# Kernel optimization log

Measured on AMD Instinct MI355X. Metric: run time of the kernel, lower is better.

Reference implementation:

```python
import jax, jax.numpy as jnp
import numpy as np

# DISTANA prediction-kernel step, fused per spatial node:
#   pre  = tanh(x @ W_pre)                       (B,N,9) -> (B,N,4)
#   net  = pre @ W_lstm + old_h                  (B,N,16) recurrent state feeds gating
#   CIFG-style LSTM cell (single gate matrix, as dictated by the (4,16) lstm_weights):
#     i        = sigmoid(net)
#     g        = tanh(net)
#     new_cell = (1-i)*old_cell + i*g
#     new_h    = tanh(new_cell)
#   y   = tanh(new_h @ W_post)                   (B,N,16) -> (B,N,9)

B, N = 128, 4096          # batch, number of prediction kernels (64x64 grid)
IN, PRE, CELLS, OUT = 9, 4, 16, 9


def setup_inputs() -> dict:
    key = jax.random.key(0)
    k = jax.random.split(key, 6)
    stdv = 1.0 / float(np.sqrt(CELLS))  # reset_parameters(): uniform(-stdv, stdv)
    return {
        "input": jax.random.normal(k[0], (B, N, IN, 1), dtype=jnp.float32),
        "pre_weights": jax.random.uniform(k[1], (IN, PRE), jnp.float32, -stdv, stdv),
        "lstm_weights": jax.random.uniform(k[2], (PRE, CELLS), jnp.float32, -stdv, stdv),
        "post_weights": jax.random.uniform(k[3], (CELLS, OUT), jnp.float32, -stdv, stdv),
        "old_h": jax.random.normal(k[4], (B, N, CELLS), dtype=jnp.float32),
        "old_cell": jax.random.normal(k[5], (B, N, CELLS), dtype=jnp.float32),
    }


def reference(input, pre_weights, lstm_weights, post_weights, old_h, old_cell):
    x = input[..., 0]                                  # (B,N,9) drop trailing singleton
    pre = jnp.tanh(jnp.einsum("bni,ip->bnp", x, pre_weights))        # (B,N,4)
    net = jnp.einsum("bnp,pc->bnc", pre, lstm_weights) + old_h       # (B,N,16)
    i = jax.nn.sigmoid(net)
    g = jnp.tanh(net)
    new_cell = (1.0 - i) * old_cell + i * g                          # (B,N,16)
    new_h = jnp.tanh(new_cell)                                       # (B,N,16)
    y = jnp.tanh(jnp.einsum("bnc,co->bno", new_h, post_weights))     # (B,N,9)
    return y, new_h, new_cell


if __name__ == "__main__":
    out = jax.jit(reference)(**setup_inputs())
    print([o.shape for o in out])
```

## Files before the change

kernel.cpp:

```cpp
#include <hip/hip_runtime.h>
#include <math.h>


#define NNODES 524288
#define IN_DIM 9
#define CELLS 16
#define OUT_DIM 9
#define TPB 256
#define NPB 64
#define NBLK (NNODES / NPB)
#define NXCD 8

typedef float f32x4 __attribute__((ext_vector_type(4)));

__device__ __forceinline__ float fast_rcp(float x) {
    return __builtin_amdgcn_rcpf(x);
}

__device__ __forceinline__ float fast_tanh(float x) {
    x = fminf(fmaxf(x, -15.f), 15.f);
    float e = __expf(2.f * x);
    return (e - 1.f) * fast_rcp(e + 1.f);
}

__device__ __forceinline__ float qsum(float v) {
    v += __int_as_float(__builtin_amdgcn_ds_swizzle(__float_as_int(v), 0x041F));
    v += __int_as_float(__builtin_amdgcn_ds_swizzle(__float_as_int(v), 0x081F));
    return v;
}

__global__ __launch_bounds__(TPB) void distana_quad_kernel(
    const float* __restrict__ input,
    const float* __restrict__ w_pre,
    const float* __restrict__ w_lstm,
    const float* __restrict__ w_post,
    const float* __restrict__ old_h,
    const float* __restrict__ old_cell,
    float* __restrict__ y,
    float* __restrict__ new_h,
    float* __restrict__ new_cell)
{
    __shared__ float sWpre[64];
    __shared__ float sWl[64];
    __shared__ float sWp[144];

    const int t   = threadIdx.x;
    const int bid = blockIdx.x;
    const int swz  = (bid & (NXCD - 1)) * (NBLK / NXCD) + (bid >> 3);
    const int node = swz * NPB + (t >> 2);
    const int sub  = t & 3;

    const float* hp = old_h    + (size_t)node * CELLS + sub * 4;
    const float* cp = old_cell + (size_t)node * CELLS + sub * 4;
    f32x4 h = *(const f32x4*)hp;
    f32x4 c = *(const f32x4*)cp;

    const float* xp = input + (size_t)node * IN_DIM;
    f32x4 xl = {0.f, 0.f, 0.f, 0.f};
    if (sub == 0)      { xl[0] = xp[0]; xl[1] = xp[1]; xl[2] = xp[2]; xl[3] = xp[3]; }
    else if (sub == 1) { xl[0] = xp[4]; xl[1] = xp[5]; xl[2] = xp[6]; xl[3] = xp[7]; }
    else if (sub == 2) { xl[0] = xp[8]; }

    if (t < 64)  sWpre[t] = (t < 36) ? w_pre[t] : 0.f;
    if (t < 64)  sWl[t]   = w_lstm[t];
    if (t < 144) sWp[t]   = w_post[t];
    __syncthreads();

    float pre[4];
    #pragma unroll
    for (int p = 0; p < 4; ++p) {
        float s = 0.f;
        #pragma unroll
        for (int k = 0; k < 4; ++k)
            s = fmaf(xl[k], sWpre[(sub * 4 + k) * 4 + p], s);
        pre[p] = fast_tanh(qsum(s));
    }

    f32x4 nh, nc;
    #pragma unroll
    for (int j = 0; j < 4; ++j) {
        const int cc = sub * 4 + j;
        float s = h[j];
        #pragma unroll
        for (int p = 0; p < 4; ++p)
            s = fmaf(pre[p], sWl[p * CELLS + cc], s);
        s = fminf(fmaxf(s, -15.f), 15.f);
        float e  = __expf(s);
        float e2 = e * e;
        float a  = 1.f + e;
        float b  = 1.f + e2;
        float r  = fast_rcp(a * b);
        float ig = e * b * r;
        float g  = (e2 - 1.f) * a * r;
        float v  = fmaf(ig, g - c[j], c[j]);
        nc[j] = v;
        nh[j] = fast_tanh(v);
    }
    *(f32x4*)(new_h    + (size_t)node * CELLS + sub * 4) = nh;
    *(f32x4*)(new_cell + (size_t)node * CELLS + sub * 4) = nc;

    float py[OUT_DIM];
    #pragma unroll
    for (int o = 0; o < OUT_DIM; ++o) {
        float s = 0.f;
        #pragma unroll
        for (int j = 0; j < 4; ++j)
            s = fmaf(nh[j], sWp[(sub * 4 + j) * OUT_DIM + o], s);
        py[o] = qsum(s);
    }
    float* yo = y + (size_t)node * OUT_DIM;
    if (sub == 0) {
        yo[0] = fast_tanh(py[0]); yo[1] = fast_tanh(py[1]);
        yo[2] = fast_tanh(py[2]); yo[3] = fast_tanh(py[3]);
    } else if (sub == 1) {
        yo[4] = fast_tanh(py[4]); yo[5] = fast_tanh(py[5]);
        yo[6] = fast_tanh(py[6]); yo[7] = fast_tanh(py[7]);
    } else if (sub == 2) {
        yo[8] = fast_tanh(py[8]);
    }
}

extern "C" void kernel_launch(void* const* d_in, const int* in_sizes, int n_in,
                              void* d_out, int out_size, void* d_ws, size_t ws_size,
                              hipStream_t stream) {
    const float* input    = (const float*)d_in[0];
    const float* w_pre    = (const float*)d_in[1];
    const float* w_lstm   = (const float*)d_in[2];
    const float* w_post   = (const float*)d_in[3];
    const float* old_h    = (const float*)d_in[4];
    const float* old_cell = (const float*)d_in[5];

    float* out = (float*)d_out;
    float* yp       = out;
    float* new_h    = out + (size_t)NNODES * OUT_DIM;
    float* new_cell = new_h + (size_t)NNODES * CELLS;

    dim3 grid(NBLK), block(TPB);
    distana_quad_kernel<<<grid, block, 0, stream>>>(
        input, w_pre, w_lstm, w_post, old_h, old_cell, yp, new_h, new_cell);
}
```

Measured before the change: 33.38 us.

## Use DPP quad reductions, nontemporal stores, drop clamps, reorder loads

Replaces ds_swizzle quad reductions with DPP row permutes, writes all outputs with nontemporal stores, and removes clamping before several exp calls. It also moves the weight loads to shared memory ahead of the global h/c loads and spreads the y writes as 3/3/3 across lanes. The aim is lower instruction latency and less cache pollution on a store-heavy, memory-bound kernel. Without the clamps, exp can overflow to inf for large inputs, and (inf-1)*rcp(inf+1) can produce NaN in tanh.

```diff
diff --git a/kernel.cpp b/kernel.cpp
--- a/kernel.cpp
+++ b/kernel.cpp
@@ -17,15 +17,20 @@
     return __builtin_amdgcn_rcpf(x);
 }
 
-__device__ __forceinline__ float fast_tanh(float x) {
-    x = fminf(fmaxf(x, -15.f), 15.f);
+__device__ __forceinline__ float tanh_nc(float x) {
     float e = __expf(2.f * x);
     return (e - 1.f) * fast_rcp(e + 1.f);
 }
 
+__device__ __forceinline__ float fast_tanh(float x) {
+    return tanh_nc(fminf(fmaxf(x, -15.f), 15.f));
+}
+
 __device__ __forceinline__ float qsum(float v) {
-    v += __int_as_float(__builtin_amdgcn_ds_swizzle(__float_as_int(v), 0x041F));
-    v += __int_as_float(__builtin_amdgcn_ds_swizzle(__float_as_int(v), 0x081F));
+    int a = __builtin_amdgcn_update_dpp(0, __float_as_int(v), 0xB1, 0xF, 0xF, true);
+    v += __int_as_float(a);
+    int b = __builtin_amdgcn_update_dpp(0, __float_as_int(v), 0x4E, 0xF, 0xF, true);
+    v += __int_as_float(b);
     return v;
 }
 
@@ -50,10 +55,9 @@
     const int node = swz * NPB + (t >> 2);
     const int sub  = t & 3;
 
-    const float* hp = old_h    + (size_t)node * CELLS + sub * 4;
-    const float* cp = old_cell + (size_t)node * CELLS + sub * 4;
-    f32x4 h = *(const f32x4*)hp;
-    f32x4 c = *(const f32x4*)cp;
+    if (t < 64)  sWpre[t] = (t < 36) ? w_pre[t] : 0.f;
+    if (t < 64)  sWl[t]   = w_lstm[t];
+    if (t < 144) sWp[t]   = w_post[t];
 
     const float* xp = input + (size_t)node * IN_DIM;
     f32x4 xl = {0.f, 0.f, 0.f, 0.f};
@@ -61,9 +65,11 @@
     else if (sub == 1) { xl[0] = xp[4]; xl[1] = xp[5]; xl[2] = xp[6]; xl[3] = xp[7]; }
     else if (sub == 2) { xl[0] = xp[8]; }
 
-    if (t < 64)  sWpre[t] = (t < 36) ? w_pre[t] : 0.f;
-    if (t < 64)  sWl[t]   = w_lstm[t];
-    if (t < 144) sWp[t]   = w_post[t];
+    const float* hp = old_h    + (size_t)node * CELLS + sub * 4;
+    const float* cp = old_cell + (size_t)node * CELLS + sub * 4;
+    f32x4 h = *(const f32x4*)hp;
+    f32x4 c = *(const f32x4*)cp;
+
     __syncthreads();
 
     float pre[4];
@@ -84,7 +90,6 @@
         #pragma unroll
         for (int p = 0; p < 4; ++p)
             s = fmaf(pre[p], sWl[p * CELLS + cc], s);
-        s = fminf(fmaxf(s, -15.f), 15.f);
         float e  = __expf(s);
         float e2 = e * e;
         float a  = 1.f + e;
@@ -94,10 +99,10 @@
         float g  = (e2 - 1.f) * a * r;
         float v  = fmaf(ig, g - c[j], c[j]);
         nc[j] = v;
-        nh[j] = fast_tanh(v);
+        nh[j] = tanh_nc(v);
     }
-    *(f32x4*)(new_h    + (size_t)node * CELLS + sub * 4) = nh;
-    *(f32x4*)(new_cell + (size_t)node * CELLS + sub * 4) = nc;
+    __builtin_nontemporal_store(nh, (f32x4*)(new_h    + (size_t)node * CELLS + sub * 4));
+    __builtin_nontemporal_store(nc, (f32x4*)(new_cell + (size_t)node * CELLS + sub * 4));
 
     float py[OUT_DIM];
     #pragma unroll
@@ -110,13 +115,17 @@
     }
     float* yo = y + (size_t)node * OUT_DIM;
     if (sub == 0) {
-        yo[0] = fast_tanh(py[0]); yo[1] = fast_tanh(py[1]);
-        yo[2] = fast_tanh(py[2]); yo[3] = fast_tanh(py[3]);
+        __builtin_nontemporal_store(tanh_nc(py[0]), yo + 0);
+        __builtin_nontemporal_store(tanh_nc(py[1]), yo + 1);
+        __builtin_nontemporal_store(tanh_nc(py[2]), yo + 2);
     } else if (sub == 1) {
-        yo[4] = fast_tanh(py[4]); yo[5] = fast_tanh(py[5]);
-        yo[6] = fast_tanh(py[6]); yo[7] = fast_tanh(py[7]);
+        __builtin_nontemporal_store(tanh_nc(py[3]), yo + 3);
+        __builtin_nontemporal_store(tanh_nc(py[4]), yo + 4);
+        __builtin_nontemporal_store(tanh_nc(py[5]), yo + 5);
     } else if (sub == 2) {
-        yo[8] = fast_tanh(py[8]);
+        __builtin_nontemporal_store(tanh_nc(py[6]), yo + 6);
+        __builtin_nontemporal_store(tanh_nc(py[7]), yo + 7);
+        __builtin_nontemporal_store(tanh_nc(py[8]), yo + 8);
     }
 }
 
```

Result: slower. 41.35 us (+23.9%).
